# Performance work log

Hardware: AMD Instinct MI355X
Metric: run time of the kernel (lower is better)

## Reference

```python
import jax, jax.numpy as jnp
import numpy as np

N = 100000
E = 3200000
F_IN, HID, C = 256, 128, 40


def setup_inputs() -> dict:
    key = jax.random.key(0)
    k1, k2, k3, k4, k5 = jax.random.split(key, 5)
    x = jax.random.normal(k1, (N, F_IN), dtype=jnp.float32)
    edge_index = jax.random.randint(k2, (2, E), 0, N, dtype=jnp.int64)
    edge_weight = jax.random.uniform(k3, (E,), dtype=jnp.float32)
    W1 = jax.random.normal(k4, (F_IN, HID), dtype=jnp.float32) * (1.0 / np.sqrt(F_IN))
    b1 = jnp.zeros((HID,), dtype=jnp.float32)
    W2 = jax.random.normal(k5, (HID, C), dtype=jnp.float32) * (1.0 / np.sqrt(HID))
    b2 = jnp.zeros((C,), dtype=jnp.float32)
    return {"x": x, "edge_index": edge_index, "edge_weight": edge_weight,
            "W1": W1, "b1": b1, "W2": W2, "b2": b2}


def gcn_conv(x, edge_index, edge_weight, W, b):
    # PyG GCNConv (add_self_loops=False, normalize=False):
    # 1) linear transform, 2) edge-weighted scatter-add from src to dst.
    h = x @ W  # [N, d_out]
    src, dst = edge_index[0], edge_index[1]
    msgs = h[src] * edge_weight[:, None]  # [E, d_out]
    agg = jax.ops.segment_sum(msgs, dst, num_segments=x.shape[0])
    return agg + b


def reference(x, edge_index, edge_weight, W1, b1, W2, b2):
    # dropout is identity in eval mode
    h = jax.nn.relu(gcn_conv(x, edge_index, edge_weight, W1, b1))
    out = gcn_conv(h, edge_index, edge_weight, W2, b2)
    return jax.nn.log_softmax(out, axis=1)
```

## Files before the change

### kernel.cpp

```cpp
#include <hip/hip_runtime.h>
#include <hip/hip_bf16.h>
#include <hip/hip_fp16.h>
#include <math.h>

#define N_NODES 100000
#define E_EDGES 3200000
#define F_INF   256
#define HIDF    128
#define C_OUT   40
#define H2P     64

#define BSH   8
#define NB    391
#define NSEG  32
#define CAP   384
#define OCAP  262144
#define EPB   1563
#define SCAT_BLOCKS 2048
#define W1T_BLOCKS  128
#define GEMM1_BLOCKS ((N_NODES + 127) / 128)

typedef __attribute__((ext_vector_type(8))) short bf16x8;
typedef __attribute__((ext_vector_type(4))) float f32x4;

static __device__ __forceinline__ short bf16c(float f) {
    __hip_bfloat16 b = __float2bfloat16(f);
    return *reinterpret_cast<short*>(&b);
}

static __device__ void scat_body(int bid, const int* __restrict__ ei,
        const float* __restrict__ ew, int* __restrict__ cnt,
        int2* __restrict__ rec, int* __restrict__ ocnt,
        int2* __restrict__ osw, int* __restrict__ odst) {
    int seg = bid & (NSEG - 1);
    int e0 = bid * EPB;
    int e1 = e0 + EPB; if (e1 > E_EDGES) e1 = E_EDGES;
    for (int e = e0 + threadIdx.x; e < e1; e += 256) {
        int dst = ei[E_EDGES + e];
        int src = ei[e];
        float w = ew[e];
        int b = dst >> BSH;
        int packed = src | ((dst & 255) << 17);
        int pos = atomicAdd(&cnt[seg * NB + b], 1);
        if (pos < CAP) {
            rec[(size_t)(seg * NB + b) * CAP + pos] =
                make_int2(packed, __float_as_int(w));
        } else {
            int op = atomicAdd(ocnt, 1);
            if (op < OCAP) { osw[op] = make_int2(src, __float_as_int(w)); odst[op] = dst; }
        }
    }
}

static __device__ void w1t_body(int bid, const float* __restrict__ W1,
                                short* __restrict__ w1t) {
    int idx = bid * 256 + threadIdx.x;
    int k = idx >> 7, c = idx & 127;
    w1t[c * 256 + k] = bf16c(W1[idx]);
}

__global__ __launch_bounds__(256) void scat_w1t_kernel(const int* __restrict__ ei,
        const float* __restrict__ ew, int* __restrict__ cnt,
        int2* __restrict__ rec, int* __restrict__ ocnt,
        int2* __restrict__ osw, int* __restrict__ odst,
        const float* __restrict__ W1, short* __restrict__ w1t) {
    if (blockIdx.x < SCAT_BLOCKS)
        scat_body(blockIdx.x, ei, ew, cnt, rec, ocnt, osw, odst);
    else
        w1t_body(blockIdx.x - SCAT_BLOCKS, W1, w1t);
}

static __device__ void csr_body(char* smem, int b, const int* __restrict__ cnt,
        const int2* __restrict__ rec, const int* __restrict__ ocnt,
        const int2* __restrict__ osw, const int* __restrict__ odst,
        int* __restrict__ rowptr, int2* __restrict__ srcw) {
    int* hist = (int*)smem;
    int* sc   = hist + 256;
    int* cur  = sc + 256;
    int* red  = cur + 256;
    int* s_base = red + 4;
    int tid = threadIdx.x;
    hist[tid] = 0;

    int partial = 0;
    for (int i = tid; i < b * NSEG; i += 256) {
        int bp = i >> 5, s = i & 31;
        int c = cnt[s * NB + bp];
        partial += (c < CAP ? c : CAP);
    }
    int onum = *ocnt; if (onum > OCAP) onum = OCAP;
    for (int i = tid; i < onum; i += 256)
        if ((odst[i] >> BSH) < b) ++partial;
    #pragma unroll
    for (int off = 32; off; off >>= 1) partial += __shfl_xor(partial, off);
    if ((tid & 63) == 0) red[tid >> 6] = partial;
    __syncthreads();
    if (tid == 0) *s_base = red[0] + red[1] + red[2] + red[3];
    __syncthreads();

    for (int s = 0; s < NSEG; ++s) {
        int c = cnt[s * NB + b]; if (c > CAP) c = CAP;
        const int2* rp = &rec[(size_t)(s * NB + b) * CAP];
        for (int i = tid; i < c; i += 256)
            atomicAdd(&hist[(rp[i].x >> 17) & 255], 1);
    }
    for (int i = tid; i < onum; i += 256) {
        int d = odst[i];
        if ((d >> BSH) == b) atomicAdd(&hist[d & 255], 1);
    }
    __syncthreads();

    sc[tid] = hist[tid];
    __syncthreads();
    for (int off = 1; off < 256; off <<= 1) {
        int v = (tid >= off) ? sc[tid - off] : 0;
        __syncthreads();
        sc[tid] += v;
        __syncthreads();
    }
    int excl = (tid > 0) ? sc[tid - 1] : 0;
    cur[tid] = excl;
    int base = *s_base;
    int node = b * 256 + tid;
    if (node <= N_NODES) rowptr[node] = base + excl;
    __syncthreads();

    for (int s = 0; s < NSEG; ++s) {
        int c = cnt[s * NB + b]; if (c > CAP) c = CAP;
        const int2* rp = &rec[(size_t)(s * NB + b) * CAP];
        for (int i = tid; i < c; i += 256) {
            int2 r = rp[i];
            int dl = (r.x >> 17) & 255;
            int p = atomicAdd(&cur[dl], 1);
            srcw[base + p] = make_int2(r.x & 0x1FFFF, r.y);
        }
    }
    for (int i = tid; i < onum; i += 256) {
        int d = odst[i];
        if ((d >> BSH) == b) {
            int p = atomicAdd(&cur[d & 255], 1);
            srcw[base + p] = osw[i];
        }
    }
}

static __device__ void gemm1_body(char* smem, int bid, const float* __restrict__ x,
                                  const short* __restrict__ w1t,
                                  __half* __restrict__ h) {
    int tid = threadIdx.x;
    int lane = tid & 63, wid = tid >> 6;
    int wr = wid >> 1, wc = wid & 1;
    int m0 = bid * 128;
    f32x4 acc[4][4] = {{{0.f}}};
    for (int kb = 0; kb < 256; kb += 64) {
        #pragma unroll
        for (int t = 0; t < 8; ++t) {
            int id = tid + t * 256;
            int row = id >> 4, c4 = id & 15;
            int gr = m0 + row; if (gr >= N_NODES) gr = N_NODES - 1;
            float4 g = *(const float4*)&x[(size_t)gr * F_INF + kb + c4 * 4];
            short4 s4 = { bf16c(g.x), bf16c(g.y), bf16c(g.z), bf16c(g.w) };
            int byte = row * 128 + c4 * 8;
            byte ^= (row & 7) << 4;
            *(short4*)(smem + byte) = s4;
        }
        __syncthreads();
        #pragma unroll
        for (int km = 0; km < 2; ++km) {
            bf16x8 af[4], bfr[4];
            #pragma unroll
            for (int mi = 0; mi < 4; ++mi) {
                int row = wr * 64 + mi * 16 + (lane & 15);
                int kk = km * 32 + (lane >> 4) * 8;
                int byte = row * 128 + kk * 2;
                byte ^= (row & 7) << 4;
                af[mi] = *(bf16x8*)(smem + byte);
            }
            #pragma unroll
            for (int ni = 0; ni < 4; ++ni) {
                int col = wc * 64 + ni * 16 + (lane & 15);
                int kk = kb + km * 32 + (lane >> 4) * 8;
                bfr[ni] = *(const bf16x8*)&w1t[col * 256 + kk];
            }
            #pragma unroll
            for (int mi = 0; mi < 4; ++mi)
                #pragma unroll
                for (int ni = 0; ni < 4; ++ni)
                    acc[mi][ni] = __builtin_amdgcn_mfma_f32_16x16x32_bf16(
                        af[mi], bfr[ni], acc[mi][ni], 0, 0, 0);
        }
        __syncthreads();
    }
    #pragma unroll
    for (int mi = 0; mi < 4; ++mi) {
        int rbase = m0 + wr * 64 + mi * 16 + ((lane >> 4) << 2);
        #pragma unroll
        for (int ni = 0; ni < 4; ++ni) {
            int col = wc * 64 + ni * 16 + (lane & 15);
            #pragma unroll
            for (int r = 0; r < 4; ++r) {
                int row = rbase + r;
                if (row < N_NODES)
                    h[(size_t)row * HIDF + col] = __float2half(acc[mi][ni][r]);
            }
        }
    }
}

__global__ __launch_bounds__(256) void csr_gemm1_kernel(const int* __restrict__ cnt,
        const int2* __restrict__ rec, const int* __restrict__ ocnt,
        const int2* __restrict__ osw, const int* __restrict__ odst,
        int* __restrict__ rowptr, int2* __restrict__ srcw,
        const float* __restrict__ x, const short* __restrict__ w1t,
        __half* __restrict__ h) {
    __shared__ char smem[16384];
    if (blockIdx.x < NB)
        csr_body(smem, blockIdx.x, cnt, rec, ocnt, osw, odst, rowptr, srcw);
    else
        gemm1_body(smem, blockIdx.x - NB, x, w1t, h);
}

__global__ __launch_bounds__(256) void agg1_kernel(const __half* __restrict__ h,
                                                   const int2* __restrict__ srcw,
                                                   const int* __restrict__ rowptr,
                                                   const float* __restrict__ b1,
                                                   __half* __restrict__ hact) {
    int lane = threadIdx.x & 63;
    int node = blockIdx.x * 4 + (threadIdx.x >> 6);
    if (node >= N_NODES) return;
    int beg = rowptr[node], end = rowptr[node + 1];
    int eo = lane >> 4, fo = lane & 15;
    float4 a0 = {0.f, 0.f, 0.f, 0.f}, a1 = {0.f, 0.f, 0.f, 0.f};
    const uint4* hp = (const uint4*)h;
    int idx0 = beg + lane;
    int2 sw = srcw[idx0 < end ? idx0 : end - 1];
    for (int base = beg; base < end; base += 64) {
        int cnt = end - base; if (cnt > 64) cnt = 64;
        int nidx = base + 64 + lane;
        int2 swn = srcw[nidx < end ? nidx : end - 1];
        for (int j = 0; j < cnt; j += 16) {
            int s[4]; float w[4];
            #pragma unroll
            for (int u = 0; u < 4; ++u) {
                int jj = j + u * 4 + eo;
                s[u] = __shfl(sw.x, jj);
                w[u] = __int_as_float(__shfl(sw.y, jj));
                if (jj >= cnt) w[u] = 0.f;
            }
            uint4 hv[4];
            #pragma unroll
            for (int u = 0; u < 4; ++u) hv[u] = hp[(size_t)s[u] * 16 + fo];
            #pragma unroll
            for (int u = 0; u < 4; ++u) {
                const __half2* p = (const __half2*)&hv[u];
                float2 f;
                f = __half22float2(p[0]); a0.x += w[u] * f.x; a0.y += w[u] * f.y;
                f = __half22float2(p[1]); a0.z += w[u] * f.x; a0.w += w[u] * f.y;
                f = __half22float2(p[2]); a1.x += w[u] * f.x; a1.y += w[u] * f.y;
                f = __half22float2(p[3]); a1.z += w[u] * f.x; a1.w += w[u] * f.y;
            }
        }
        sw = swn;
    }
    #pragma unroll
    for (int off = 16; off < 64; off <<= 1) {
        a0.x += __shfl_xor(a0.x, off); a0.y += __shfl_xor(a0.y, off);
        a0.z += __shfl_xor(a0.z, off); a0.w += __shfl_xor(a0.w, off);
        a1.x += __shfl_xor(a1.x, off); a1.y += __shfl_xor(a1.y, off);
        a1.z += __shfl_xor(a1.z, off); a1.w += __shfl_xor(a1.w, off);
    }
    if (lane < 16) {
        float4 bb0 = *(const float4*)&b1[fo * 8];
        float4 bb1 = *(const float4*)&b1[fo * 8 + 4];
        __half2 o0 = __floats2half2_rn(fmaxf(a0.x + bb0.x, 0.f), fmaxf(a0.y + bb0.y, 0.f));
        __half2 o1 = __floats2half2_rn(fmaxf(a0.z + bb0.z, 0.f), fmaxf(a0.w + bb0.w, 0.f));
        __half2 o2 = __floats2half2_rn(fmaxf(a1.x + bb1.x, 0.f), fmaxf(a1.y + bb1.y, 0.f));
        __half2 o3 = __floats2half2_rn(fmaxf(a1.z + bb1.z, 0.f), fmaxf(a1.w + bb1.w, 0.f));
        uint4 ov = { *(uint*)&o0, *(uint*)&o1, *(uint*)&o2, *(uint*)&o3 };
        ((uint4*)hact)[(size_t)node * 16 + fo] = ov;
    }
}

__global__ __launch_bounds__(320) void gemm2_kernel(const __half* __restrict__ hact,
                                                    const float* __restrict__ W2,
                                                    __half* __restrict__ h2p) {
    __shared__ float xT[128 * 68];
    __shared__ float w2[128 * 40];
    int tid = threadIdx.x;
    int tx = tid % 40, ty = tid / 40;
    int m0 = blockIdx.x * 64;
    for (int i = tid; i < 128 * 40; i += 320) w2[i] = W2[i];
    for (int i = tid; i < 1024; i += 320) {
        int row = i >> 4, c8 = i & 15;
        int gr = m0 + row; if (gr >= N_NODES) gr = N_NODES - 1;
        uint4 v = *(const uint4*)&hact[(size_t)gr * HIDF + c8 * 8];
        const __half2* ph = (const __half2*)&v;
        #pragma unroll
        for (int t = 0; t < 4; ++t) {
            float2 f = __half22float2(ph[t]);
            int k = c8 * 8 + t * 2;
            xT[(k + 0) * 68 + row] = f.x;
            xT[(k + 1) * 68 + row] = f.y;
        }
    }
    for (int i = tid; i < 64 * 3; i += 320) {
        int row = i / 3, c = i % 3;
        int gr = m0 + row;
        if (gr < N_NODES) {
            uint4 z = {0, 0, 0, 0};
            *(uint4*)&h2p[(size_t)gr * H2P + 40 + c * 8] = z;
        }
    }
    __syncthreads();
    float acc[8] = {};
    #pragma unroll 4
    for (int k = 0; k < 128; ++k) {
        float wv = w2[k * 40 + tx];
        float4 xa = *(float4*)&xT[k * 68 + ty * 8];
        float4 xb = *(float4*)&xT[k * 68 + ty * 8 + 4];
        acc[0] += xa.x * wv; acc[1] += xa.y * wv;
        acc[2] += xa.z * wv; acc[3] += xa.w * wv;
        acc[4] += xb.x * wv; acc[5] += xb.y * wv;
        acc[6] += xb.z * wv; acc[7] += xb.w * wv;
    }
    #pragma unroll
    for (int i = 0; i < 8; ++i) {
        int r = m0 + ty * 8 + i;
        if (r < N_NODES) h2p[(size_t)r * H2P + tx] = __float2half(acc[i]);
    }
}

__global__ __launch_bounds__(256) void agg2_kernel(const __half* __restrict__ h2p,
                                                   const int2* __restrict__ srcw,
                                                   const int* __restrict__ rowptr,
                                                   const float* __restrict__ b2,
                                                   float* __restrict__ out) {
    int lane = threadIdx.x & 63;
    int node = blockIdx.x * 4 + (threadIdx.x >> 6);
    if (node >= N_NODES) return;
    int beg = rowptr[node], end = rowptr[node + 1];
    int eo = lane >> 3, fo = lane & 7;
    float4 a0 = {0.f, 0.f, 0.f, 0.f}, a1 = {0.f, 0.f, 0.f, 0.f};
    const uint4* hp = (const uint4*)h2p;
    int idx0 = beg + lane;
    int2 sw = srcw[idx0 < end ? idx0 : end - 1];
    for (int base = beg; base < end; base += 64) {
        int cnt = end - base; if (cnt > 64) cnt = 64;
        int nidx = base + 64 + lane;
        int2 swn = srcw[nidx < end ? nidx : end - 1];
        for (int j = 0; j < cnt; j += 16) {
            int s[2]; float w[2];
            #pragma unroll
            for (int u = 0; u < 2; ++u) {
                int jj = j + u * 8 + eo;
                s[u] = __shfl(sw.x, jj);
                w[u] = __int_as_float(__shfl(sw.y, jj));
                if (jj >= cnt) w[u] = 0.f;
            }
            uint4 hv[2];
            #pragma unroll
            for (int u = 0; u < 2; ++u) hv[u] = hp[(size_t)s[u] * 8 + fo];
            #pragma unroll
            for (int u = 0; u < 2; ++u) {
                const __half2* p = (const __half2*)&hv[u];
                float2 f;
                f = __half22float2(p[0]); a0.x += w[u] * f.x; a0.y += w[u] * f.y;
                f = __half22float2(p[1]); a0.z += w[u] * f.x; a0.w += w[u] * f.y;
                f = __half22float2(p[2]); a1.x += w[u] * f.x; a1.y += w[u] * f.y;
                f = __half22float2(p[3]); a1.z += w[u] * f.x; a1.w += w[u] * f.y;
            }
        }
        sw = swn;
    }
    #pragma unroll
    for (int off = 8; off < 64; off <<= 1) {
        a0.x += __shfl_xor(a0.x, off); a0.y += __shfl_xor(a0.y, off);
        a0.z += __shfl_xor(a0.z, off); a0.w += __shfl_xor(a0.w, off);
        a1.x += __shfl_xor(a1.x, off); a1.y += __shfl_xor(a1.y, off);
        a1.z += __shfl_xor(a1.z, off); a1.w += __shfl_xor(a1.w, off);
    }
    float v[8];
    bool act = (lane < 8) && (fo < 5);
    #pragma unroll
    for (int t = 0; t < 8; ++t) v[t] = -INFINITY;
    if (act) {
        float4 bb0 = *(const float4*)&b2[fo * 8];
        float4 bb1 = *(const float4*)&b2[fo * 8 + 4];
        v[0] = a0.x + bb0.x; v[1] = a0.y + bb0.y;
        v[2] = a0.z + bb0.z; v[3] = a0.w + bb0.w;
        v[4] = a1.x + bb1.x; v[5] = a1.y + bb1.y;
        v[6] = a1.z + bb1.z; v[7] = a1.w + bb1.w;
    }
    float m = v[0];
    #pragma unroll
    for (int t = 1; t < 8; ++t) m = fmaxf(m, v[t]);
    #pragma unroll
    for (int off = 1; off < 8; off <<= 1) m = fmaxf(m, __shfl_xor(m, off));
    float ex = 0.f;
    if (act) {
        #pragma unroll
        for (int t = 0; t < 8; ++t) ex += expf(v[t] - m);
    }
    #pragma unroll
    for (int off = 1; off < 8; off <<= 1) ex += __shfl_xor(ex, off);
    float ls = logf(ex);
    if (act) {
        float4 o0 = { v[0]-m-ls, v[1]-m-ls, v[2]-m-ls, v[3]-m-ls };
        float4 o1 = { v[4]-m-ls, v[5]-m-ls, v[6]-m-ls, v[7]-m-ls };
        *(float4*)&out[(size_t)node * C_OUT + fo * 8] = o0;
        *(float4*)&out[(size_t)node * C_OUT + fo * 8 + 4] = o1;
    }
}


extern "C" void kernel_launch(void* const* d_in, const int* in_sizes, int n_in,
                              void* d_out, int out_size, void* d_ws, size_t ws_size,
                              hipStream_t stream) {
    const float* x  = (const float*)d_in[0];
    const int*   ei = (const int*)d_in[1];
    const float* ew = (const float*)d_in[2];
    const float* W1 = (const float*)d_in[3];
    const float* b1 = (const float*)d_in[4];
    const float* W2 = (const float*)d_in[5];
    const float* b2 = (const float*)d_in[6];
    float* out = (float*)d_out;

    char* ws = (char*)d_ws;
    size_t off = 0;
    auto alloc = [&](size_t bytes) -> void* {
        void* p = ws + off;
        off += (bytes + 255) & ~(size_t)255;
        return p;
    };
    __half* h      = (__half*)alloc((size_t)N_NODES * HIDF * 2);
    __half* hact   = (__half*)alloc((size_t)N_NODES * HIDF * 2);
    __half* h2p    = (__half*)alloc((size_t)N_NODES * H2P * 2);
    short*  w1t    = (short*)alloc((size_t)HIDF * F_INF * 2);
    int*    rowptr = (int*)alloc((size_t)(N_NODES + 1) * 4);
    int2*   srcw   = (int2*)alloc((size_t)E_EDGES * 8);
    int2*   rec    = (int2*)alloc((size_t)NSEG * NB * CAP * 8);
    int*    cnt    = (int*)alloc((size_t)NSEG * NB * 4);
    int*    ocnt   = (int*)alloc(256);
    int2*   osw    = (int2*)alloc((size_t)OCAP * 8);
    int*    odst   = (int*)alloc((size_t)OCAP * 4);

    hipMemsetAsync(cnt, 0, (size_t)NSEG * NB * 4, stream);
    hipMemsetAsync(ocnt, 0, 4, stream);

    scat_w1t_kernel<<<SCAT_BLOCKS + W1T_BLOCKS, 256, 0, stream>>>(
        ei, ew, cnt, rec, ocnt, osw, odst, W1, w1t);
    csr_gemm1_kernel<<<NB + GEMM1_BLOCKS, 256, 0, stream>>>(
        cnt, rec, ocnt, osw, odst, rowptr, srcw, x, w1t, h);
    agg1_kernel<<<(N_NODES + 3) / 4, 256, 0, stream>>>(h, srcw, rowptr, b1, hact);
    gemm2_kernel<<<(N_NODES + 63) / 64, 320, 0, stream>>>(hact, W2, h2p);
    agg2_kernel<<<(N_NODES + 3) / 4, 256, 0, stream>>>(h2p, srcw, rowptr, b2, out);
}
```

Before: 548.4 us.

## Bucket edges in LDS per block before writing coalesced runs to global bins

The scatter phase now counts edges per destination bucket in shared memory, prefix-sums the counts, and reserves a contiguous range in each global bin with one atomic per bucket per block instead of one global atomic per edge. Edges are staged in an LDS buffer ordered by bucket and then written to the record array in contiguous runs. The number of segments drops from 32 to 8 with larger per-bin capacity, which the CSR pass is updated to match. This adds LDS usage and several block-wide barriers and scans to the scatter kernel, and that LDS is also allocated for the W1-transpose blocks.

```diff
diff --git a/kernel.cpp b/kernel.cpp
--- a/kernel.cpp
+++ b/kernel.cpp
@@ -12,13 +12,15 @@
 
 #define BSH   8
 #define NB    391
-#define NSEG  32
-#define CAP   384
+#define NSEG  8
+#define CAPX  1280
 #define OCAP  262144
 #define EPB   1563
+#define BUFSZ 1568
 #define SCAT_BLOCKS 2048
 #define W1T_BLOCKS  128
 #define GEMM1_BLOCKS ((N_NODES + 127) / 128)
+#define SCAT_LDS    26112
 
 typedef __attribute__((ext_vector_type(8))) short bf16x8;
 typedef __attribute__((ext_vector_type(4))) float f32x4;
@@ -28,26 +30,85 @@
     return *reinterpret_cast<short*>(&b);
 }
 
-static __device__ void scat_body(int bid, const int* __restrict__ ei,
+static __device__ void scat_body(char* smem, int bid, const int* __restrict__ ei,
         const float* __restrict__ ew, int* __restrict__ cnt,
         int2* __restrict__ rec, int* __restrict__ ocnt,
         int2* __restrict__ osw, int* __restrict__ odst) {
+    int* hist  = (int*)smem;
+    int* g     = hist + 392;
+    int* lcur  = g + 256;
+    int* gsA   = lcur + 392;
+    int* lim   = gsA + 392;
+    int2* buf  = (int2*)(lim + 392);
+    int* gdest = (int*)(buf + BUFSZ);
+    int tid = threadIdx.x;
     int seg = bid & (NSEG - 1);
     int e0 = bid * EPB;
     int e1 = e0 + EPB; if (e1 > E_EDGES) e1 = E_EDGES;
-    for (int e = e0 + threadIdx.x; e < e1; e += 256) {
-        int dst = ei[E_EDGES + e];
-        int src = ei[e];
-        float w = ew[e];
-        int b = dst >> BSH;
-        int packed = src | ((dst & 255) << 17);
-        int pos = atomicAdd(&cnt[seg * NB + b], 1);
-        if (pos < CAP) {
-            rec[(size_t)(seg * NB + b) * CAP + pos] =
-                make_int2(packed, __float_as_int(w));
+    int tot = e1 - e0;
+
+    for (int i = tid; i < 392; i += 256) hist[i] = 0;
+    __syncthreads();
+
+    int pk[7]; float wv[7]; int bk[7]; int nr = 0;
+    #pragma unroll
+    for (int r = 0; r < 7; ++r) {
+        int e = e0 + r * 256 + tid;
+        if (e < e1) {
+            int dst = __builtin_nontemporal_load(&ei[E_EDGES + e]);
+            int src = __builtin_nontemporal_load(&ei[e]);
+            float w = __builtin_nontemporal_load(&ew[e]);
+            int b = dst >> BSH;
+            pk[nr] = src | ((dst & 255) << 17);
+            wv[nr] = w; bk[nr] = b; ++nr;
+            atomicAdd(&hist[b], 1);
+        }
+    }
+    __syncthreads();
+
+    int h0 = (2 * tid < 392) ? hist[2 * tid] : 0;
+    int h1 = (2 * tid + 1 < 392) ? hist[2 * tid + 1] : 0;
+    g[tid] = h0 + h1;
+    __syncthreads();
+    for (int off = 1; off < 256; off <<= 1) {
+        int v = (tid >= off) ? g[tid - off] : 0;
+        __syncthreads();
+        g[tid] += v;
+        __syncthreads();
+    }
+    int pg = (tid > 0) ? g[tid - 1] : 0;
+    if (2 * tid < 392)     lcur[2 * tid] = pg;
+    if (2 * tid + 1 < 392) lcur[2 * tid + 1] = pg + h0;
+    __syncthreads();
+
+    for (int b = tid; b < NB; b += 256) {
+        int c = hist[b];
+        int gb = 0;
+        if (c > 0) gb = atomicAdd(&cnt[seg * NB + b], c);
+        int lb = lcur[b];
+        gsA[b] = (seg * NB + b) * CAPX + gb - lb;
+        lim[b] = lb + (CAPX - gb);
+    }
+    __syncthreads();
+
+    for (int r = 0; r < nr; ++r) {
+        int b = bk[r];
+        int p = atomicAdd(&lcur[b], 1);
+        buf[p] = make_int2(pk[r], __float_as_int(wv[r]));
+        gdest[p] = (p < lim[b]) ? (gsA[b] + p) : -(b + 1);
+    }
+    __syncthreads();
+
+    for (int i = tid; i < tot; i += 256) {
+        int d = gdest[i];
+        int2 rr = buf[i];
+        if (d >= 0) {
+            rec[d] = rr;
         } else {
+            int b = -d - 1;
+            int dst = (b << 8) | ((rr.x >> 17) & 255);
             int op = atomicAdd(ocnt, 1);
-            if (op < OCAP) { osw[op] = make_int2(src, __float_as_int(w)); odst[op] = dst; }
+            if (op < OCAP) { osw[op] = make_int2(rr.x & 0x1FFFF, rr.y); odst[op] = dst; }
         }
     }
 }
@@ -64,8 +125,9 @@
         int2* __restrict__ rec, int* __restrict__ ocnt,
         int2* __restrict__ osw, int* __restrict__ odst,
         const float* __restrict__ W1, short* __restrict__ w1t) {
+    __shared__ char smem[SCAT_LDS];
     if (blockIdx.x < SCAT_BLOCKS)
-        scat_body(blockIdx.x, ei, ew, cnt, rec, ocnt, osw, odst);
+        scat_body(smem, blockIdx.x, ei, ew, cnt, rec, ocnt, osw, odst);
     else
         w1t_body(blockIdx.x - SCAT_BLOCKS, W1, w1t);
 }
@@ -84,9 +146,9 @@
 
     int partial = 0;
     for (int i = tid; i < b * NSEG; i += 256) {
-        int bp = i >> 5, s = i & 31;
+        int bp = i >> 3, s = i & 7;
         int c = cnt[s * NB + bp];
-        partial += (c < CAP ? c : CAP);
+        partial += (c < CAPX ? c : CAPX);
     }
     int onum = *ocnt; if (onum > OCAP) onum = OCAP;
     for (int i = tid; i < onum; i += 256)
@@ -99,8 +161,8 @@
     __syncthreads();
 
     for (int s = 0; s < NSEG; ++s) {
-        int c = cnt[s * NB + b]; if (c > CAP) c = CAP;
-        const int2* rp = &rec[(size_t)(s * NB + b) * CAP];
+        int c = cnt[s * NB + b]; if (c > CAPX) c = CAPX;
+        const int2* rp = &rec[(size_t)(s * NB + b) * CAPX];
         for (int i = tid; i < c; i += 256)
             atomicAdd(&hist[(rp[i].x >> 17) & 255], 1);
     }
@@ -126,8 +188,8 @@
     __syncthreads();
 
     for (int s = 0; s < NSEG; ++s) {
-        int c = cnt[s * NB + b]; if (c > CAP) c = CAP;
-        const int2* rp = &rec[(size_t)(s * NB + b) * CAP];
+        int c = cnt[s * NB + b]; if (c > CAPX) c = CAPX;
+        const int2* rp = &rec[(size_t)(s * NB + b) * CAPX];
         for (int i = tid; i < c; i += 256) {
             int2 r = rp[i];
             int dl = (r.x >> 17) & 255;
@@ -438,7 +500,7 @@
     short*  w1t    = (short*)alloc((size_t)HIDF * F_INF * 2);
     int*    rowptr = (int*)alloc((size_t)(N_NODES + 1) * 4);
     int2*   srcw   = (int2*)alloc((size_t)E_EDGES * 8);
-    int2*   rec    = (int2*)alloc((size_t)NSEG * NB * CAP * 8);
+    int2*   rec    = (int2*)alloc((size_t)NSEG * NB * CAPX * 8);
     int*    cnt    = (int*)alloc((size_t)NSEG * NB * 4);
     int*    ocnt   = (int*)alloc(256);
     int2*   osw    = (int2*)alloc((size_t)OCAP * 8);
```

New measurement: 484.5 us. -11.7%, faster.
